# Optimization experiments

Measured on AMD Instinct MI355X. Metric: run time of the kernel, lower is better.

## Reference

```python
import jax, jax.numpy as jnp
import numpy as np

C = 256
SQ = C // 4  # squeeze_channels

def hardsigmoid(v):
    # torch Hardsigmoid: relu6(v + 3) / 6
    return jnp.clip(v / 6.0 + 0.5, 0.0, 1.0)

def setup_inputs() -> dict:
    key = jax.random.key(0)
    k1, k2, k3, k4, k5 = jax.random.split(key, 5)
    x = jax.random.normal(k1, (32, C, 64, 64), dtype=jnp.float32)
    # Conv2d 1x1 weights stored as [out, in] (kernel dims squeezed)
    s1 = 1.0 / np.sqrt(C)
    s2 = 1.0 / np.sqrt(SQ)
    W1 = jax.random.uniform(k2, (SQ, C), jnp.float32, -s1, s1)
    b1 = jax.random.uniform(k3, (SQ,), jnp.float32, -s1, s1)
    W2 = jax.random.uniform(k4, (C, SQ), jnp.float32, -s2, s2)
    b2 = jax.random.uniform(k5, (C,), jnp.float32, -s2, s2)
    return {"x": x, "W1": W1, "b1": b1, "W2": W2, "b2": b2}

def reference(x, W1, b1, W2, b2):
    # fc1 (1x1 conv) applied on full spatial map, then mean over (H, W)
    # scale: [B, SQ, H, W] -> mean -> [B, SQ]
    s = jnp.einsum('bchw,oc->bohw', x, W1) + b1[None, :, None, None]
    s = s.mean(axis=(2, 3))                      # [B, SQ]
    s = jax.nn.relu(s)
    s = jnp.einsum('bo,co->bc', s, W2) + b2      # [B, C]
    gate = hardsigmoid(s)[:, :, None, None]      # [B, C, 1, 1]
    return x * gate
```

## Files before the change

kernel.cpp:

```cpp
#include <hip/hip_runtime.h>


#define SE_B  32
#define SE_C  256
#define SE_SQ 64
#define SE_HW 4096
#define CHUNK 16

typedef float f32x4 __attribute__((ext_vector_type(4)));

__device__ __forceinline__ float hsig(float v) {
    return fminf(fmaxf(v * (1.0f / 6.0f) + 0.5f, 0.0f), 1.0f);
}

__global__ __launch_bounds__(256) void se_mean_kernel(
    const float* __restrict__ x, float* __restrict__ m) {
    const int bc = blockIdx.x;
    const int t  = threadIdx.x;
    const f32x4* xv = reinterpret_cast<const f32x4*>(x) + (size_t)bc * (SE_HW / 4);

    float s = 0.0f;
#pragma unroll
    for (int k = 0; k < 4; ++k) {
        f32x4 v = xv[t + 256 * k];
        s += (v.x + v.y) + (v.z + v.w);
    }
#pragma unroll
    for (int off = 32; off > 0; off >>= 1) s += __shfl_down(s, off);

    __shared__ float wsum[4];
    if ((t & 63) == 0) wsum[t >> 6] = s;
    __syncthreads();
    if (t == 0) m[bc] = (wsum[0] + wsum[1] + wsum[2] + wsum[3]) * (1.0f / SE_HW);
}

__global__ __launch_bounds__(1024, 8) void se_gate_scale_kernel(
    const float* __restrict__ x, const float* __restrict__ m,
    const float* __restrict__ W1, const float* __restrict__ b1,
    const float* __restrict__ W2, const float* __restrict__ b2,
    float* __restrict__ y) {
    const int b     = blockIdx.x >> 4;
    const int chunk = blockIdx.x & 15;
    const int c0    = chunk * CHUNK;
    const int t     = threadIdx.x;
    const int wave  = t >> 6;
    const int lane  = t & 63;

    __shared__ f32x4 m4_lds[SE_C / 4];
    __shared__ float s_lds[SE_SQ];
    __shared__ float g_lds[CHUNK];

    if (t < SE_C / 4)
        m4_lds[t] = reinterpret_cast<const f32x4*>(m + b * SE_C)[t];
    __syncthreads();

    const f32x4* W1v = reinterpret_cast<const f32x4*>(W1);
    const f32x4 mv = m4_lds[lane];
#pragma unroll
    for (int i = 0; i < 4; ++i) {
        const int o = wave * 4 + i;
        f32x4 w4 = W1v[o * 64 + lane];
        float p = w4.x * mv.x;
        p = fmaf(w4.y, mv.y, p);
        p = fmaf(w4.z, mv.z, p);
        p = fmaf(w4.w, mv.w, p);
#pragma unroll
        for (int off = 1; off < 64; off <<= 1) p += __shfl_xor(p, off);
        if (lane == 0) s_lds[o] = fmaxf(p + b1[o], 0.0f);
    }
    __syncthreads();

    {
        const int c = c0 + wave;
        float p = W2[c * SE_SQ + lane] * s_lds[lane];
#pragma unroll
        for (int off = 1; off < 64; off <<= 1) p += __shfl_xor(p, off);
        if (lane == 0) g_lds[wave] = hsig(p + b2[c]);
    }
    __syncthreads();

    const size_t base = ((size_t)b * SE_C + c0) * (SE_HW / 4);
    const f32x4* xv = reinterpret_cast<const f32x4*>(x) + base;
    f32x4*       yv = reinterpret_cast<f32x4*>(y)       + base;
#pragma unroll 4
    for (int j = 0; j < CHUNK; ++j) {
        const float g = g_lds[j];
        f32x4 v = xv[j * (SE_HW / 4) + t];
        v *= g;
        __builtin_nontemporal_store(v, &yv[j * (SE_HW / 4) + t]);
    }
}

extern "C" void kernel_launch(void* const* d_in, const int* in_sizes, int n_in,
                              void* d_out, int out_size, void* d_ws, size_t ws_size,
                              hipStream_t stream) {
    const float* x  = (const float*)d_in[0];
    const float* W1 = (const float*)d_in[1];
    const float* b1 = (const float*)d_in[2];
    const float* W2 = (const float*)d_in[3];
    const float* b2 = (const float*)d_in[4];
    float* y = (float*)d_out;

    float* m = (float*)d_ws;

    se_mean_kernel<<<SE_B * SE_C, 256, 0, stream>>>(x, m);
    se_gate_scale_kernel<<<SE_B * (SE_C / CHUNK), 1024, 0, stream>>>(
        x, m, W1, b1, W2, b2, y);
}
```

Baseline: 69.94 us.

## Fuse mean and gate-scale into one kernel with per-batch spin barrier

The separate mean and gate/scale kernels are merged into one persistent-style kernel. Each block loads its 16 channels once, holding most of the data in registers and LDS while computing channel means. Blocks of the same batch then synchronise through a global atomic counter, and the kept data is scaled and written back, so x is mostly read once instead of twice. The cost is heavy register and LDS use, plus a spin-wait that relies on all 16 blocks of a batch being resident at once, which risks deadlock or stalls. A memset is also added each call.

```diff
diff --git a/kernel.cpp b/kernel.cpp
--- a/kernel.cpp
+++ b/kernel.cpp
@@ -5,7 +5,13 @@
 #define SE_C  256
 #define SE_SQ 64
 #define SE_HW 4096
-#define CHUNK 16
+#define CPB   16
+#define TPB   512
+#define VPT   32
+#define N_RE  5
+#define N_LDS 7
+#define N_REG 20
+#define RDY_STRIDE 32
 
 typedef float f32x4 __attribute__((ext_vector_type(4)));
 
@@ -13,42 +19,63 @@
     return fminf(fmaxf(v * (1.0f / 6.0f) + 0.5f, 0.0f), 1.0f);
 }
 
-__global__ __launch_bounds__(256) void se_mean_kernel(
-    const float* __restrict__ x, float* __restrict__ m) {
-    const int bc = blockIdx.x;
-    const int t  = threadIdx.x;
-    const f32x4* xv = reinterpret_cast<const f32x4*>(x) + (size_t)bc * (SE_HW / 4);
-
-    float s = 0.0f;
-#pragma unroll
-    for (int k = 0; k < 4; ++k) {
-        f32x4 v = xv[t + 256 * k];
-        s += (v.x + v.y) + (v.z + v.w);
-    }
-#pragma unroll
-    for (int off = 32; off > 0; off >>= 1) s += __shfl_down(s, off);
-
-    __shared__ float wsum[4];
-    if ((t & 63) == 0) wsum[t >> 6] = s;
-    __syncthreads();
-    if (t == 0) m[bc] = (wsum[0] + wsum[1] + wsum[2] + wsum[3]) * (1.0f / SE_HW);
-}
-
-__global__ __launch_bounds__(1024, 8) void se_gate_scale_kernel(
-    const float* __restrict__ x, const float* __restrict__ m,
+__global__ __launch_bounds__(TPB, 4) void se_fused_kernel(
+    const float* __restrict__ x,
     const float* __restrict__ W1, const float* __restrict__ b1,
     const float* __restrict__ W2, const float* __restrict__ b2,
+    float* __restrict__ m, int* __restrict__ ready,
     float* __restrict__ y) {
-    const int b     = blockIdx.x >> 4;
-    const int chunk = blockIdx.x & 15;
-    const int c0    = chunk * CHUNK;
-    const int t     = threadIdx.x;
-    const int wave  = t >> 6;
-    const int lane  = t & 63;
+    const int blk  = blockIdx.x;
+    const int b    = blk >> 4;
+    const int c0   = (blk & 15) * CPB;
+    const int t    = threadIdx.x;
+    const int wave = t >> 6;
+    const int lane = t & 63;
 
+    __shared__ f32x4 ldsdata[N_LDS * TPB];
+    __shared__ float partials[CPB * 8];
     __shared__ f32x4 m4_lds[SE_C / 4];
     __shared__ float s_lds[SE_SQ];
-    __shared__ float g_lds[CHUNK];
+    __shared__ float g_lds[CPB];
+
+    const size_t base = ((size_t)b * SE_C + c0) * (SE_HW / 4);
+    const f32x4* xv = reinterpret_cast<const f32x4*>(x) + base;
+    f32x4*       yv = reinterpret_cast<f32x4*>(y)       + base;
+
+    f32x4 keep[N_REG];
+    float part = 0.0f;
+#pragma unroll
+    for (int k = 0; k < VPT; ++k) {
+        f32x4 v = xv[k * TPB + t];
+        if (k >= N_RE && k < N_RE + N_LDS) ldsdata[(k - N_RE) * TPB + t] = v;
+        if (k >= N_RE + N_LDS)             keep[k - (N_RE + N_LDS)] = v;
+        part += (v.x + v.y) + (v.z + v.w);
+        if (k & 1) {
+            float p = part;
+#pragma unroll
+            for (int off = 1; off < 64; off <<= 1) p += __shfl_xor(p, off);
+            if (lane == 0) partials[(k >> 1) * 8 + wave] = p;
+            part = 0.0f;
+        }
+    }
+    __syncthreads();
+
+    if (t < CPB) {
+        float s = 0.0f;
+#pragma unroll
+        for (int w = 0; w < 8; ++w) s += partials[t * 8 + w];
+        m[b * SE_C + c0 + t] = s * (1.0f / SE_HW);
+    }
+    __syncthreads();
+
+    if (t == 0) {
+        __hip_atomic_fetch_add(&ready[b * RDY_STRIDE], 1,
+                               __ATOMIC_RELEASE, __HIP_MEMORY_SCOPE_AGENT);
+        while (__hip_atomic_load(&ready[b * RDY_STRIDE],
+                                 __ATOMIC_ACQUIRE, __HIP_MEMORY_SCOPE_AGENT) < CPB)
+            __builtin_amdgcn_s_sleep(2);
+    }
+    __syncthreads();
 
     if (t < SE_C / 4)
         m4_lds[t] = reinterpret_cast<const f32x4*>(m + b * SE_C)[t];
@@ -57,8 +84,8 @@
     const f32x4* W1v = reinterpret_cast<const f32x4*>(W1);
     const f32x4 mv = m4_lds[lane];
 #pragma unroll
-    for (int i = 0; i < 4; ++i) {
-        const int o = wave * 4 + i;
+    for (int i = 0; i < 8; ++i) {
+        const int o = wave * 8 + i;
         f32x4 w4 = W1v[o * 64 + lane];
         float p = w4.x * mv.x;
         p = fmaf(w4.y, mv.y, p);
@@ -70,24 +97,26 @@
     }
     __syncthreads();
 
-    {
-        const int c = c0 + wave;
+#pragma unroll
+    for (int i = 0; i < 2; ++i) {
+        const int cl = wave * 2 + i;
+        const int c  = c0 + cl;
         float p = W2[c * SE_SQ + lane] * s_lds[lane];
 #pragma unroll
         for (int off = 1; off < 64; off <<= 1) p += __shfl_xor(p, off);
-        if (lane == 0) g_lds[wave] = hsig(p + b2[c]);
+        if (lane == 0) g_lds[cl] = hsig(p + b2[c]);
     }
     __syncthreads();
 
-    const size_t base = ((size_t)b * SE_C + c0) * (SE_HW / 4);
-    const f32x4* xv = reinterpret_cast<const f32x4*>(x) + base;
-    f32x4*       yv = reinterpret_cast<f32x4*>(y)       + base;
-#pragma unroll 4
-    for (int j = 0; j < CHUNK; ++j) {
-        const float g = g_lds[j];
-        f32x4 v = xv[j * (SE_HW / 4) + t];
+#pragma unroll
+    for (int k = 0; k < VPT; ++k) {
+        const float g = g_lds[k >> 1];
+        f32x4 v;
+        if (k < N_RE)                 v = xv[k * TPB + t];
+        else if (k < N_RE + N_LDS)    v = ldsdata[(k - N_RE) * TPB + t];
+        else                          v = keep[k - (N_RE + N_LDS)];
         v *= g;
-        __builtin_nontemporal_store(v, &yv[j * (SE_HW / 4) + t]);
+        __builtin_nontemporal_store(v, &yv[k * TPB + t]);
     }
 }
 
@@ -101,9 +130,10 @@
     const float* b2 = (const float*)d_in[4];
     float* y = (float*)d_out;
 
-    float* m = (float*)d_ws;
+    float* m     = (float*)d_ws;
+    int*   ready = (int*)(m + SE_B * SE_C);
 
-    se_mean_kernel<<<SE_B * SE_C, 256, 0, stream>>>(x, m);
-    se_gate_scale_kernel<<<SE_B * (SE_C / CHUNK), 1024, 0, stream>>>(
-        x, m, W1, b1, W2, b2, y);
+    hipMemsetAsync(ready, 0, SE_B * RDY_STRIDE * sizeof(int), stream);
+    se_fused_kernel<<<SE_B * (SE_C / CPB), TPB, 0, stream>>>(
+        x, W1, b1, W2, b2, m, ready, y);
 }
```

Measured after the change: 72.50 us. 1.04x slower.
